# Performance work log

Hardware: AMD Instinct MI355X
Metric: run time of the kernel (lower is better)

Reference implementation:

```python
import jax, jax.numpy as jnp
import numpy as np

B, T, H, E = 256, 256, 512, 96  # batch, enc seq len, hidden/enc dim, charset size


def setup_inputs() -> dict:
    key = jax.random.key(0)
    ks = jax.random.split(key, 9)
    s = 0.05  # param scale
    return {
        "prev_h": jax.random.normal(ks[0], (B, H), jnp.float32),
        "prev_c": jax.random.normal(ks[1], (B, H), jnp.float32),
        "batch_H": jax.random.normal(ks[2], (B, T, H), jnp.float32),
        "char_onehots": jax.nn.one_hot(jax.random.randint(ks[3], (B,), 0, E), E, dtype=jnp.float32),
        "W_i2h": jax.random.normal(ks[4], (H, H), jnp.float32) * s,
        "W_h2h": jax.random.normal(ks[5], (H, H), jnp.float32) * s,
        "b_h2h": jnp.zeros((H,), jnp.float32),
        "w_score": jax.random.normal(ks[6], (H, 1), jnp.float32) * s,
        "W_lstm": jax.random.normal(ks[7], (H + E, 4 * H), jnp.float32) * s,
        "U_lstm": jax.random.normal(ks[8], (H, 4 * H), jnp.float32) * s,
        "b_lstm": jnp.zeros((4 * H,), jnp.float32),
    }


def reference(prev_h, prev_c, batch_H, char_onehots,
              W_i2h, W_h2h, b_h2h, w_score, W_lstm, U_lstm, b_lstm):
    # Additive (Bahdanau) attention
    proj = jnp.einsum('btd,dh->bth', batch_H, W_i2h)          # [B,T,H]
    hp = prev_h @ W_h2h + b_h2h                               # [B,H]
    e = jnp.tanh(proj + hp[:, None, :]) @ w_score             # [B,T,1]
    alpha = jax.nn.softmax(e, axis=1)                         # [B,T,1]
    context = jnp.einsum('bt,btd->bd', alpha[..., 0], batch_H)  # [B,D]
    x = jnp.concatenate([context, char_onehots], axis=1)      # [B,D+E]
    # Keras LSTMCell: gate order i, f, c(g), o
    z = x @ W_lstm + prev_h @ U_lstm + b_lstm                 # [B,4H]
    i, f, g, o = jnp.split(z, 4, axis=1)
    c_new = jax.nn.sigmoid(f) * prev_c + jax.nn.sigmoid(i) * jnp.tanh(g)
    h_new = jax.nn.sigmoid(o) * jnp.tanh(c_new)
    return h_new, c_new, alpha
```

## Files before the change

kernel.cpp:

```cpp
#include <hip/hip_runtime.h>
#include <hip/hip_bf16.h>
#include <math.h>

#define Bq 256
#define Tq 256
#define Hq 512
#define Eq 96

typedef __attribute__((ext_vector_type(8))) short short8;
typedef __attribute__((ext_vector_type(4))) float f32x4;

static __device__ __forceinline__ unsigned short f2bf(float f) {
  union { float f; unsigned u; } v; v.f = f;
  unsigned r = v.u + 0x7FFF + ((v.u >> 16) & 1);
  return (unsigned short)(r >> 16);
}

static __device__ __forceinline__ ushort4 pack4(float4 v) {
  ushort4 p;
  p.x = f2bf(v.x); p.y = f2bf(v.y); p.z = f2bf(v.z); p.w = f2bf(v.w);
  return p;
}

static __device__ __forceinline__ float sat_tanh(float x) {
  float ax = fminf(fabsf(x), 15.0f);
  float e = __builtin_exp2f(ax * 2.885390082f);
  float t = 1.0f - 2.0f / (e + 1.0f);
  return copysignf(t, x);
}

static __device__ __forceinline__ float sat_sig(float x) {
  float cx = fmaxf(fminf(x, 30.0f), -30.0f);
  return 1.0f / (1.0f + __builtin_exp2f(-cx * 1.442695041f));
}

__global__ __launch_bounds__(256) void convW_k(const float* __restrict__ W,
                                               unsigned short* __restrict__ Wt) {
  __shared__ float tile[32][33];
  int bx = blockIdx.x & 15, by = blockIdx.x >> 4;
  int tx = threadIdx.x & 31, ty = threadIdx.x >> 5;
  #pragma unroll
  for (int i = 0; i < 32; i += 8)
    tile[ty + i][tx] = W[(size_t)(by * 32 + ty + i) * Hq + bx * 32 + tx];
  __syncthreads();
  #pragma unroll
  for (int i = 0; i < 32; i += 8)
    Wt[(size_t)(bx * 32 + ty + i) * Hq + by * 32 + tx] = f2bf(tile[tx][ty + i]);
}

__global__ __launch_bounds__(256) void hsplit_k(const float* __restrict__ ph,
                                                const float* __restrict__ Whh,
                                                float* __restrict__ hp) {
  __shared__ __align__(16) float xs[8][128];
  const int ks = blockIdx.x & 3;
  const int nc = (blockIdx.x >> 2) & 3;
  const int bg = blockIdx.x >> 4;
  const int tid = threadIdx.x;
  const int row0 = bg * 8;
  const int d0 = ks * 128;
  for (int i = tid; i < 8 * 32; i += 256) {
    int r = i >> 5, dd = (i & 31) * 4;
    *(float4*)&xs[r][dd] = *(const float4*)&ph[(size_t)(row0 + r) * Hq + d0 + dd];
  }
  __syncthreads();
  const int rt = tid >> 6;
  const int ct = tid & 63;
  const int n = nc * 128 + ct * 2;
  float a00 = 0, a01 = 0, a10 = 0, a11 = 0;
  for (int dd = 0; dd < 128; dd += 4) {
    float4 x0 = *(const float4*)&xs[rt * 2][dd];
    float4 x1 = *(const float4*)&xs[rt * 2 + 1][dd];
    #pragma unroll
    for (int j = 0; j < 4; j++) {
      float2 w = *(const float2*)&Whh[(size_t)(d0 + dd + j) * Hq + n];
      float xj0 = ((const float*)&x0)[j];
      float xj1 = ((const float*)&x1)[j];
      a00 += xj0 * w.x; a01 += xj0 * w.y;
      a10 += xj1 * w.x; a11 += xj1 * w.y;
    }
  }
  int row = row0 + rt * 2;
  atomicAdd(&hp[(size_t)row * Hq + n], a00);
  atomicAdd(&hp[(size_t)row * Hq + n + 1], a01);
  atomicAdd(&hp[(size_t)(row + 1) * Hq + n], a10);
  atomicAdd(&hp[(size_t)(row + 1) * Hq + n + 1], a11);
}

#define LDKA 520

__global__ __launch_bounds__(512, 2) void fused_score3_k(
    const float* __restrict__ A,
    const unsigned short* __restrict__ Wt,
    const float* __restrict__ hp,
    const float* __restrict__ bh,
    const float* __restrict__ wsc,
    float* __restrict__ e) {
  __shared__ unsigned short As[64 * LDKA];
  __shared__ float red[8][64];

  const int tid = threadIdx.x;
  const int m0 = blockIdx.x * 64;
  const int b = m0 >> 8;
  const int wave = tid >> 6;
  const int lane = tid & 63;
  const int quad = lane >> 4;
  const int l16 = lane & 15;
  const int wn = wave * 64;

  {
    const int sr = tid >> 3;
    const int sc = (tid & 7) * 64;
    const float* Ar = A + (size_t)(m0 + sr) * Hq + sc;
    unsigned short* dst = &As[sr * LDKA + sc];
    #pragma unroll
    for (int j = 0; j < 64; j += 8) {
      float4 v0 = *(const float4*)&Ar[j];
      float4 v1 = *(const float4*)&Ar[j + 4];
      *(ushort4*)&dst[j] = pack4(v0);
      *(ushort4*)&dst[j + 4] = pack4(v1);
    }
  }
  __syncthreads();

  f32x4 acc[4][4] = {};
  const unsigned short* Bp = Wt + (size_t)(wn + l16) * Hq + quad * 8;
  const unsigned short* Ap = &As[l16 * LDKA + quad * 8];

  #pragma unroll 4
  for (int ks = 0; ks < 16; ks++) {
    const int k0 = ks * 32;
    short8 af[4];
    #pragma unroll
    for (int mi = 0; mi < 4; mi++)
      af[mi] = *(const short8*)(Ap + mi * 16 * LDKA + k0);
    #pragma unroll
    for (int ni = 0; ni < 4; ni++) {
      short8 bf = *(const short8*)(Bp + (size_t)ni * 16 * Hq + k0);
      #pragma unroll
      for (int mi = 0; mi < 4; mi++)
        acc[mi][ni] = __builtin_amdgcn_mfma_f32_16x16x32_bf16(
            af[mi], bf, acc[mi][ni], 0, 0, 0);
    }
  }

  float hv[4], wv[4];
  #pragma unroll
  for (int ni = 0; ni < 4; ni++) {
    int c = wn + ni * 16 + l16;
    hv[ni] = hp[(size_t)b * Hq + c] + bh[c];
    wv[ni] = wsc[c];
  }
  #pragma unroll
  for (int mi = 0; mi < 4; mi++) {
    float s[4] = {0, 0, 0, 0};
    #pragma unroll
    for (int ni = 0; ni < 4; ni++)
      #pragma unroll
      for (int r = 0; r < 4; r++)
        s[r] += sat_tanh(acc[mi][ni][r] + hv[ni]) * wv[ni];
    #pragma unroll
    for (int r = 0; r < 4; r++) {
      s[r] += __shfl_xor(s[r], 8, 64);
      s[r] += __shfl_xor(s[r], 4, 64);
      s[r] += __shfl_xor(s[r], 2, 64);
      s[r] += __shfl_xor(s[r], 1, 64);
    }
    if (l16 == 0) {
      #pragma unroll
      for (int r = 0; r < 4; r++) red[wave][mi * 16 + quad * 4 + r] = s[r];
    }
  }
  __syncthreads();
  if (tid < 64) {
    float t = 0.f;
    #pragma unroll
    for (int w = 0; w < 8; w++) t += red[w][tid];
    e[m0 + tid] = t;
  }
}

__global__ __launch_bounds__(256) void softmax_k(float* __restrict__ ea) {
  __shared__ float red[8];
  int b = blockIdx.x, t = threadIdx.x;
  int wave = t >> 6, lane = t & 63;
  float x = ea[b * Tq + t];
  float m = x;
  #pragma unroll
  for (int off = 32; off >= 1; off >>= 1) m = fmaxf(m, __shfl_xor(m, off, 64));
  if (lane == 0) red[wave] = m;
  __syncthreads();
  m = fmaxf(fmaxf(red[0], red[1]), fmaxf(red[2], red[3]));
  float ex = __builtin_exp2f((x - m) * 1.442695041f);
  float s = ex;
  #pragma unroll
  for (int off = 32; off >= 1; off >>= 1) s += __shfl_xor(s, off, 64);
  if (lane == 0) red[4 + wave] = s;
  __syncthreads();
  s = red[4] + red[5] + red[6] + red[7];
  ea[b * Tq + t] = ex / s;
}

__global__ __launch_bounds__(256) void ctxsplit_k(const float* __restrict__ alpha,
                                                  const float* __restrict__ bH,
                                                  float* __restrict__ ctx) {
  __shared__ float al[64];
  const int b = blockIdx.x >> 2;
  const int tc = blockIdx.x & 3;
  const int tid = threadIdx.x;
  if (tid < 64) al[tid] = alpha[b * Tq + tc * 64 + tid];
  __syncthreads();
  const float2* Hp = (const float2*)(bH + (size_t)b * Tq * Hq + (size_t)tc * 64 * Hq);
  float ax = 0.f, ay = 0.f;
  #pragma unroll 8
  for (int t = 0; t < 64; t++) {
    float a = al[t];
    float2 v = Hp[t * (Hq / 2) + tid];
    ax += a * v.x;
    ay += a * v.y;
  }
  atomicAdd(&ctx[(size_t)b * Hq + 2 * tid], ax);
  atomicAdd(&ctx[(size_t)b * Hq + 2 * tid + 1], ay);
}

__global__ __launch_bounds__(256) void zsplit_k(
    const float* __restrict__ ctx, const float* __restrict__ oneh,
    const float* __restrict__ ph, const float* __restrict__ Wl,
    const float* __restrict__ Ul, float* __restrict__ z) {
  __shared__ __align__(16) float xs[8 * 280];
  const int ks = blockIdx.x & 3;
  const int hc = (blockIdx.x >> 2) & 7;
  const int bg = blockIdx.x >> 5;
  const int tid = threadIdx.x;
  const int row0 = bg * 8;
  const int dbase = ks * 280;

  for (int i = tid; i < 8 * 280; i += 256) {
    int r = i / 280, dd = i % 280;
    int g = dbase + dd;
    float v;
    if (g < 512) v = ctx[(size_t)(row0 + r) * Hq + g];
    else if (g < 608) v = oneh[(row0 + r) * Eq + (g - 512)];
    else v = ph[(size_t)(row0 + r) * Hq + (g - 608)];
    xs[r * 280 + dd] = v;
  }
  __syncthreads();

  const int rt = tid >> 6;
  const int ct = tid & 63;
  const int c0 = ct * 4;
  const int gate = c0 >> 6;
  const int ho = c0 & 63;
  const int n = gate * 512 + hc * 64 + ho;

  float acc0[4] = {0, 0, 0, 0};
  float acc1[4] = {0, 0, 0, 0};
  const float* xr0 = &xs[(rt * 2) * 280];
  const float* xr1 = &xs[(rt * 2 + 1) * 280];

  for (int dd = 0; dd < 280; dd += 4) {
    float4 x0 = *(const float4*)&xr0[dd];
    float4 x1 = *(const float4*)&xr1[dd];
    #pragma unroll
    for (int j = 0; j < 4; j++) {
      int d = dbase + dd + j;
      const float* wp = (d < 608) ? &Wl[(size_t)d * 2048 + n]
                                  : &Ul[(size_t)(d - 608) * 2048 + n];
      float4 w = *(const float4*)wp;
      float a = ((const float*)&x0)[j], b = ((const float*)&x1)[j];
      acc0[0] += a * w.x; acc0[1] += a * w.y; acc0[2] += a * w.z; acc0[3] += a * w.w;
      acc1[0] += b * w.x; acc1[1] += b * w.y; acc1[2] += b * w.z; acc1[3] += b * w.w;
    }
  }
  const int r0 = row0 + rt * 2;
  #pragma unroll
  for (int j = 0; j < 4; j++) {
    atomicAdd(&z[(size_t)r0 * 2048 + n + j], acc0[j]);
    atomicAdd(&z[(size_t)(r0 + 1) * 2048 + n + j], acc1[j]);
  }
}

__global__ __launch_bounds__(256) void gatesz_k(const float* __restrict__ z,
                                                const float* __restrict__ bl,
                                                const float* __restrict__ pc,
                                                float* __restrict__ outh,
                                                float* __restrict__ outc) {
  int p = blockIdx.x * 256 + threadIdx.x;
  #pragma unroll
  for (int q = 0; q < 2; q++, p += 65536) {
    int r = p >> 9, h = p & 511;
    const float* zb = z + (size_t)r * 2048;
    float gi = zb[h] + bl[h];
    float gf = zb[512 + h] + bl[512 + h];
    float gg = zb[1024 + h] + bl[1024 + h];
    float go = zb[1536 + h] + bl[1536 + h];
    float cn = sat_sig(gf) * pc[p] + sat_sig(gi) * sat_tanh(gg);
    float hn = sat_sig(go) * sat_tanh(cn);
    outh[p] = hn;
    outc[p] = cn;
  }
}

#define KXc 1120
__global__ __launch_bounds__(256) void zgates2_k(
    const float* __restrict__ ctx, const float* __restrict__ oneh,
    const float* __restrict__ ph, const float* __restrict__ pc,
    const float* __restrict__ Wl, const float* __restrict__ Ul,
    const float* __restrict__ bl,
    float* __restrict__ outh, float* __restrict__ outc) {
  __shared__ __align__(16) float xs[8 * KXc];
  const int bg = blockIdx.x >> 3;
  const int hc = blockIdx.x & 7;
  const int tid = threadIdx.x;
  const int row0 = bg * 8;

  for (int i = tid; i < 8 * 128; i += 256) {
    int r = i >> 7, dd = (i & 127) * 4;
    *(float4*)&xs[r * KXc + dd] = *(const float4*)&ctx[(size_t)(row0 + r) * Hq + dd];
  }
  for (int i = tid; i < 8 * 128; i += 256) {
    int r = i >> 7, dd = (i & 127) * 4;
    *(float4*)&xs[r * KXc + 608 + dd] = *(const float4*)&ph[(size_t)(row0 + r) * Hq + dd];
  }
  if (tid < 8 * 24) {
    int r = tid / 24, dd = (tid % 24) * 4;
    *(float4*)&xs[r * KXc + 512 + dd] = *(const float4*)&oneh[(row0 + r) * Eq + dd];
  }
  __syncthreads();

  const int rt = tid >> 6;
  const int ct = tid & 63;
  const int c0 = ct * 4;
  const int gate = c0 >> 6;
  const int ho = c0 & 63;
  const int n = gate * 512 + hc * 64 + ho;

  float acc0[4] = {0, 0, 0, 0};
  float acc1[4] = {0, 0, 0, 0};
  const float* xr0 = &xs[(rt * 2) * KXc];
  const float* xr1 = &xs[(rt * 2 + 1) * KXc];

  for (int d = 0; d < 608; d += 4) {
    float4 x0 = *(const float4*)&xr0[d];
    float4 x1 = *(const float4*)&xr1[d];
    #pragma unroll
    for (int j = 0; j < 4; j++) {
      float4 w = *(const float4*)&Wl[(size_t)(d + j) * 2048 + n];
      float a = ((const float*)&x0)[j], b = ((const float*)&x1)[j];
      acc0[0] += a * w.x; acc0[1] += a * w.y; acc0[2] += a * w.z; acc0[3] += a * w.w;
      acc1[0] += b * w.x; acc1[1] += b * w.y; acc1[2] += b * w.z; acc1[3] += b * w.w;
    }
  }
  for (int d = 0; d < 512; d += 4) {
    float4 x0 = *(const float4*)&xr0[608 + d];
    float4 x1 = *(const float4*)&xr1[608 + d];
    #pragma unroll
    for (int j = 0; j < 4; j++) {
      float4 w = *(const float4*)&Ul[(size_t)(d + j) * 2048 + n];
      float a = ((const float*)&x0)[j], b = ((const float*)&x1)[j];
      acc0[0] += a * w.x; acc0[1] += a * w.y; acc0[2] += a * w.z; acc0[3] += a * w.w;
      acc1[0] += b * w.x; acc1[1] += b * w.y; acc1[2] += b * w.z; acc1[3] += b * w.w;
    }
  }

  __syncthreads();
  float* zs = xs;
  #pragma unroll
  for (int j = 0; j < 4; j++) {
    zs[(rt * 2) * 256 + c0 + j] = acc0[j];
    zs[(rt * 2 + 1) * 256 + c0 + j] = acc1[j];
  }
  __syncthreads();

  #pragma unroll
  for (int p = tid; p < 512; p += 256) {
    int r = p >> 6, o = p & 63;
    int h = hc * 64 + o;
    int grow = row0 + r;
    float gi = zs[r * 256 + o]       + bl[h];
    float gf = zs[r * 256 + 64 + o]  + bl[512 + h];
    float gg = zs[r * 256 + 128 + o] + bl[1024 + h];
    float go = zs[r * 256 + 192 + o] + bl[1536 + h];
    float cn = sat_sig(gf) * pc[(size_t)grow * Hq + h] + sat_sig(gi) * sat_tanh(gg);
    float hn = sat_sig(go) * sat_tanh(cn);
    outh[(size_t)grow * Hq + h] = hn;
    outc[(size_t)grow * Hq + h] = cn;
  }
}

extern "C" void kernel_launch(void* const* d_in, const int* in_sizes, int n_in,
                              void* d_out, int out_size, void* d_ws, size_t ws_size,
                              hipStream_t stream) {
  const float* prev_h = (const float*)d_in[0];
  const float* prev_c = (const float*)d_in[1];
  const float* batch_H = (const float*)d_in[2];
  const float* oneh = (const float*)d_in[3];
  const float* W_i2h = (const float*)d_in[4];
  const float* W_h2h = (const float*)d_in[5];
  const float* b_h2h = (const float*)d_in[6];
  const float* w_score = (const float*)d_in[7];
  const float* W_lstm = (const float*)d_in[8];
  const float* U_lstm = (const float*)d_in[9];
  const float* b_lstm = (const float*)d_in[10];

  float* out = (float*)d_out;
  float* outh = out;
  float* outc = out + Bq * Hq;
  float* alpha = out + 2 * Bq * Hq;

  float* ws = (float*)d_ws;
  float* hp = ws;
  float* ctx = ws;
  unsigned short* Wt = (unsigned short*)(ws + 131072);
  float* z = ws + 131072;

  const bool bigws = ws_size >= 2621440;

  hipMemsetAsync(hp, 0, Bq * Hq * sizeof(float), stream);
  convW_k<<<256, 256, 0, stream>>>(W_i2h, Wt);
  hsplit_k<<<512, 256, 0, stream>>>(prev_h, W_h2h, hp);
  fused_score3_k<<<1024, 512, 0, stream>>>(batch_H, Wt, hp, b_h2h, w_score, alpha);
  softmax_k<<<256, 256, 0, stream>>>(alpha);
  if (bigws) {
    hipMemsetAsync(ws, 0, 2621440, stream);
    ctxsplit_k<<<1024, 256, 0, stream>>>(alpha, batch_H, ctx);
    zsplit_k<<<1024, 256, 0, stream>>>(ctx, oneh, prev_h, W_lstm, U_lstm, z);
    gatesz_k<<<256, 256, 0, stream>>>(z, b_lstm, prev_c, outh, outc);
  } else {
    hipMemsetAsync(ctx, 0, Bq * Hq * sizeof(float), stream);
    ctxsplit_k<<<1024, 256, 0, stream>>>(alpha, batch_H, ctx);
    zgates2_k<<<256, 256, 0, stream>>>(ctx, oneh, prev_h, prev_c,
                                       W_lstm, U_lstm, b_lstm, outh, outc);
  }
}
```

Baseline: 403.1 us.

## Retile attention score GEMM with double-buffered LDS tiles and enlarge zsplit row tiles

The score GEMM moves from 64-row blocks that read Wt straight from global memory to 128x256 tiles. Both A and Wt are staged through double-buffered LDS with 32-wide k-steps, and the next tile is prefetched while MFMAs run. Because each block now covers half of the N dimension, partial scores are combined with atomicAdd into alpha, which now needs a memset first. ctxsplit switches to float4 loads with a split over time steps, and zsplit processes 32 rows per block with 4 rows per thread, reusing each loaded weight vector across more rows. The costs are more atomics, an extra memset, and more block syncs.

```diff
diff --git a/kernel.cpp b/kernel.cpp
--- a/kernel.cpp
+++ b/kernel.cpp
@@ -86,67 +86,82 @@
   atomicAdd(&hp[(size_t)(row + 1) * Hq + n + 1], a11);
 }
 
-#define LDKA 520
-
-__global__ __launch_bounds__(512, 2) void fused_score3_k(
+#define LDK4 40
+
+__global__ __launch_bounds__(1024, 4) void fused_score4_k(
     const float* __restrict__ A,
     const unsigned short* __restrict__ Wt,
     const float* __restrict__ hp,
     const float* __restrict__ bh,
     const float* __restrict__ wsc,
     float* __restrict__ e) {
-  __shared__ unsigned short As[64 * LDKA];
-  __shared__ float red[8][64];
+  __shared__ unsigned short As[2][128 * LDK4];
+  __shared__ unsigned short Bs[2][256 * LDK4];
+  __shared__ float red[8][128];
 
   const int tid = threadIdx.x;
-  const int m0 = blockIdx.x * 64;
+  const int n0 = blockIdx.x * 256;
+  const int m0 = blockIdx.y * 128;
   const int b = m0 >> 8;
   const int wave = tid >> 6;
   const int lane = tid & 63;
   const int quad = lane >> 4;
   const int l16 = lane & 15;
-  const int wn = wave * 64;
+  const int wm = wave >> 3;
+  const int wn8 = wave & 7;
+
+  const int ar = tid >> 3, ac = (tid & 7) * 4;
+  const int bc = tid >> 2, bk = (tid & 3) * 8;
+  const float* Agp = A + (size_t)(m0 + ar) * Hq + ac;
+  const unsigned short* Bgp = Wt + (size_t)(n0 + bc) * Hq + bk;
+
+  f32x4 acc[4][2] = {};
 
   {
-    const int sr = tid >> 3;
-    const int sc = (tid & 7) * 64;
-    const float* Ar = A + (size_t)(m0 + sr) * Hq + sc;
-    unsigned short* dst = &As[sr * LDKA + sc];
-    #pragma unroll
-    for (int j = 0; j < 64; j += 8) {
-      float4 v0 = *(const float4*)&Ar[j];
-      float4 v1 = *(const float4*)&Ar[j + 4];
-      *(ushort4*)&dst[j] = pack4(v0);
-      *(ushort4*)&dst[j + 4] = pack4(v1);
-    }
-  }
-  __syncthreads();
-
-  f32x4 acc[4][4] = {};
-  const unsigned short* Bp = Wt + (size_t)(wn + l16) * Hq + quad * 8;
-  const unsigned short* Ap = &As[l16 * LDKA + quad * 8];
-
-  #pragma unroll 4
+    float4 a0 = *(const float4*)Agp;
+    uint4 b0 = *(const uint4*)Bgp;
+    *(ushort4*)&As[0][ar * LDK4 + ac] = pack4(a0);
+    *(uint4*)&Bs[0][bc * LDK4 + bk] = b0;
+  }
+  __syncthreads();
+
+  int cur = 0;
+  #pragma unroll 2
   for (int ks = 0; ks < 16; ks++) {
-    const int k0 = ks * 32;
-    short8 af[4];
+    float4 an;
+    uint4 bn;
+    if (ks < 15) {
+      an = *(const float4*)(Agp + (ks + 1) * 32);
+      bn = *(const uint4*)(Bgp + (ks + 1) * 32);
+    }
+
+    short8 af[4], bf[2];
     #pragma unroll
     for (int mi = 0; mi < 4; mi++)
-      af[mi] = *(const short8*)(Ap + mi * 16 * LDKA + k0);
-    #pragma unroll
-    for (int ni = 0; ni < 4; ni++) {
-      short8 bf = *(const short8*)(Bp + (size_t)ni * 16 * Hq + k0);
+      af[mi] = *(const short8*)&As[cur][(wm * 64 + mi * 16 + l16) * LDK4 + quad * 8];
+    #pragma unroll
+    for (int ni = 0; ni < 2; ni++)
+      bf[ni] = *(const short8*)&Bs[cur][(wn8 * 32 + ni * 16 + l16) * LDK4 + quad * 8];
+
+    #pragma unroll
+    for (int mi = 0; mi < 4; mi++)
       #pragma unroll
-      for (int mi = 0; mi < 4; mi++)
+      for (int ni = 0; ni < 2; ni++)
         acc[mi][ni] = __builtin_amdgcn_mfma_f32_16x16x32_bf16(
-            af[mi], bf, acc[mi][ni], 0, 0, 0);
-    }
-  }
-
-  float hv[4], wv[4];
-  #pragma unroll
-  for (int ni = 0; ni < 4; ni++) {
-    int c = wn + ni * 16 + l16;
+            af[mi], bf[ni], acc[mi][ni], 0, 0, 0);
+
+    if (ks < 15) {
+      *(ushort4*)&As[cur ^ 1][ar * LDK4 + ac] = pack4(an);
+      *(uint4*)&Bs[cur ^ 1][bc * LDK4 + bk] = bn;
+    }
+    __syncthreads();
+    cur ^= 1;
+  }
+
+  float hv[2], wv[2];
+  #pragma unroll
+  for (int ni = 0; ni < 2; ni++) {
+    int c = n0 + wn8 * 32 + ni * 16 + l16;
     hv[ni] = hp[(size_t)b * Hq + c] + bh[c];
     wv[ni] = wsc[c];
   }
@@ -154,7 +169,7 @@
   for (int mi = 0; mi < 4; mi++) {
     float s[4] = {0, 0, 0, 0};
     #pragma unroll
-    for (int ni = 0; ni < 4; ni++)
+    for (int ni = 0; ni < 2; ni++)
       #pragma unroll
       for (int r = 0; r < 4; r++)
         s[r] += sat_tanh(acc[mi][ni][r] + hv[ni]) * wv[ni];
@@ -167,15 +182,16 @@
     }
     if (l16 == 0) {
       #pragma unroll
-      for (int r = 0; r < 4; r++) red[wave][mi * 16 + quad * 4 + r] = s[r];
-    }
-  }
-  __syncthreads();
-  if (tid < 64) {
+      for (int r = 0; r < 4; r++)
+        red[wn8][wm * 64 + mi * 16 + quad * 4 + r] = s[r];
+    }
+  }
+  __syncthreads();
+  if (tid < 128) {
     float t = 0.f;
     #pragma unroll
-    for (int w = 0; w < 8; w++) t += red[w][tid];
-    e[m0 + tid] = t;
+    for (int w8 = 0; w8 < 8; w8++) t += red[w8][tid];
+    atomicAdd(&e[m0 + tid], t);
   }
 }
 
@@ -209,32 +225,36 @@
   const int tid = threadIdx.x;
   if (tid < 64) al[tid] = alpha[b * Tq + tc * 64 + tid];
   __syncthreads();
-  const float2* Hp = (const float2*)(bH + (size_t)b * Tq * Hq + (size_t)tc * 64 * Hq);
-  float ax = 0.f, ay = 0.f;
+  const float* Hp = bH + (size_t)b * Tq * Hq + (size_t)tc * 64 * Hq;
+  const int h4 = (tid & 127) * 4;
+  const int t0 = (tid >> 7) * 32;
+  float a0 = 0.f, a1 = 0.f, a2 = 0.f, a3 = 0.f;
   #pragma unroll 8
-  for (int t = 0; t < 64; t++) {
-    float a = al[t];
-    float2 v = Hp[t * (Hq / 2) + tid];
-    ax += a * v.x;
-    ay += a * v.y;
-  }
-  atomicAdd(&ctx[(size_t)b * Hq + 2 * tid], ax);
-  atomicAdd(&ctx[(size_t)b * Hq + 2 * tid + 1], ay);
-}
-
-__global__ __launch_bounds__(256) void zsplit_k(
+  for (int t = 0; t < 32; t++) {
+    float a = al[t0 + t];
+    float4 v = *(const float4*)&Hp[(size_t)(t0 + t) * Hq + h4];
+    a0 += a * v.x; a1 += a * v.y; a2 += a * v.z; a3 += a * v.w;
+  }
+  float* cp = &ctx[(size_t)b * Hq + h4];
+  atomicAdd(cp + 0, a0);
+  atomicAdd(cp + 1, a1);
+  atomicAdd(cp + 2, a2);
+  atomicAdd(cp + 3, a3);
+}
+
+__global__ __launch_bounds__(512) void zsplit_k(
     const float* __restrict__ ctx, const float* __restrict__ oneh,
     const float* __restrict__ ph, const float* __restrict__ Wl,
     const float* __restrict__ Ul, float* __restrict__ z) {
-  __shared__ __align__(16) float xs[8 * 280];
+  __shared__ float xs[32 * 280];
   const int ks = blockIdx.x & 3;
   const int hc = (blockIdx.x >> 2) & 7;
   const int bg = blockIdx.x >> 5;
   const int tid = threadIdx.x;
-  const int row0 = bg * 8;
+  const int row0 = bg * 32;
   const int dbase = ks * 280;
 
-  for (int i = tid; i < 8 * 280; i += 256) {
+  for (int i = tid; i < 32 * 280; i += 512) {
     int r = i / 280, dd = i % 280;
     int g = dbase + dd;
     float v;
@@ -252,30 +272,25 @@
   const int ho = c0 & 63;
   const int n = gate * 512 + hc * 64 + ho;
 
-  float acc0[4] = {0, 0, 0, 0};
-  float acc1[4] = {0, 0, 0, 0};
-  const float* xr0 = &xs[(rt * 2) * 280];
-  const float* xr1 = &xs[(rt * 2 + 1) * 280];
-
-  for (int dd = 0; dd < 280; dd += 4) {
-    float4 x0 = *(const float4*)&xr0[dd];
-    float4 x1 = *(const float4*)&xr1[dd];
-    #pragma unroll
-    for (int j = 0; j < 4; j++) {
-      int d = dbase + dd + j;
-      const float* wp = (d < 608) ? &Wl[(size_t)d * 2048 + n]
-                                  : &Ul[(size_t)(d - 608) * 2048 + n];
-      float4 w = *(const float4*)wp;
-      float a = ((const float*)&x0)[j], b = ((const float*)&x1)[j];
-      acc0[0] += a * w.x; acc0[1] += a * w.y; acc0[2] += a * w.z; acc0[3] += a * w.w;
-      acc1[0] += b * w.x; acc1[1] += b * w.y; acc1[2] += b * w.z; acc1[3] += b * w.w;
-    }
-  }
-  const int r0 = row0 + rt * 2;
-  #pragma unroll
-  for (int j = 0; j < 4; j++) {
-    atomicAdd(&z[(size_t)r0 * 2048 + n + j], acc0[j]);
-    atomicAdd(&z[(size_t)(r0 + 1) * 2048 + n + j], acc1[j]);
+  float acc[4][4] = {};
+  #pragma unroll 4
+  for (int dd = 0; dd < 280; dd++) {
+    int g = dbase + dd;
+    const float* wp = (g < 608) ? &Wl[(size_t)g * 2048 + n]
+                                : &Ul[(size_t)(g - 608) * 2048 + n];
+    float4 w = *(const float4*)wp;
+    #pragma unroll
+    for (int r = 0; r < 4; r++) {
+      float x = xs[(rt * 4 + r) * 280 + dd];
+      acc[r][0] += x * w.x; acc[r][1] += x * w.y;
+      acc[r][2] += x * w.z; acc[r][3] += x * w.w;
+    }
+  }
+  #pragma unroll
+  for (int r = 0; r < 4; r++) {
+    float* zp = &z[(size_t)(row0 + rt * 4 + r) * 2048 + n];
+    #pragma unroll
+    for (int j = 0; j < 4; j++) atomicAdd(zp + j, acc[r][j]);
   }
 }
 
@@ -415,15 +430,17 @@
 
   const bool bigws = ws_size >= 2621440;
 
+  hipMemsetAsync(alpha, 0, Bq * Tq * sizeof(float), stream);
   hipMemsetAsync(hp, 0, Bq * Hq * sizeof(float), stream);
   convW_k<<<256, 256, 0, stream>>>(W_i2h, Wt);
   hsplit_k<<<512, 256, 0, stream>>>(prev_h, W_h2h, hp);
-  fused_score3_k<<<1024, 512, 0, stream>>>(batch_H, Wt, hp, b_h2h, w_score, alpha);
+  dim3 g4(2, 512);
+  fused_score4_k<<<g4, 1024, 0, stream>>>(batch_H, Wt, hp, b_h2h, w_score, alpha);
   softmax_k<<<256, 256, 0, stream>>>(alpha);
   if (bigws) {
     hipMemsetAsync(ws, 0, 2621440, stream);
     ctxsplit_k<<<1024, 256, 0, stream>>>(alpha, batch_H, ctx);
-    zsplit_k<<<1024, 256, 0, stream>>>(ctx, oneh, prev_h, W_lstm, U_lstm, z);
+    zsplit_k<<<256, 512, 0, stream>>>(ctx, oneh, prev_h, W_lstm, U_lstm, z);
     gatesz_k<<<256, 256, 0, stream>>>(z, b_lstm, prev_c, outh, outc);
   } else {
     hipMemsetAsync(ctx, 0, Bq * Hq * sizeof(float), stream);
```

After: 435.2 us. 7.9% more time.

## Retile score GEMM into double-buffered 128x128 tiles and widen zsplit rows

Applied to the files above, without the earlier changes.

The attention score kernel now uses a 2D grid of 128x128 output tiles. A and B are staged through double-buffered shared memory with 64-wide K steps, and the next K slice is prefetched while the current one runs on MFMA. Partial scores across the four N tiles are combined with atomicAdd into a pre-zeroed alpha buffer, which needs an extra memset. The LSTM z kernel now computes 8 rows per thread instead of 2, so each weight load is reused more and the grid shrinks fourfold, at the cost of more registers and shared memory.

```diff
diff --git a/kernel.cpp b/kernel.cpp
--- a/kernel.cpp
+++ b/kernel.cpp
@@ -20,6 +20,12 @@
   ushort4 p;
   p.x = f2bf(v.x); p.y = f2bf(v.y); p.z = f2bf(v.z); p.w = f2bf(v.w);
   return p;
+}
+
+static __device__ __forceinline__ short8 pack8(float4 a, float4 b) {
+  union { short8 s; ushort4 u[2]; } r;
+  r.u[0] = pack4(a); r.u[1] = pack4(b);
+  return r.s;
 }
 
 static __device__ __forceinline__ float sat_tanh(float x) {
@@ -86,67 +92,95 @@
   atomicAdd(&hp[(size_t)(row + 1) * Hq + n + 1], a11);
 }
 
-#define LDKA 520
-
-__global__ __launch_bounds__(512, 2) void fused_score3_k(
+#define LDKA 72
+
+__global__ __launch_bounds__(512) void fused_score5_k(
     const float* __restrict__ A,
     const unsigned short* __restrict__ Wt,
     const float* __restrict__ hp,
     const float* __restrict__ bh,
     const float* __restrict__ wsc,
     float* __restrict__ e) {
-  __shared__ unsigned short As[64 * LDKA];
+  __shared__ unsigned short As[2][128 * LDKA];
+  __shared__ unsigned short Bs[2][128 * LDKA];
   __shared__ float red[8][64];
 
   const int tid = threadIdx.x;
-  const int m0 = blockIdx.x * 64;
+  const int n0 = blockIdx.x * 128;
+  const int m0 = blockIdx.y * 128;
   const int b = m0 >> 8;
   const int wave = tid >> 6;
   const int lane = tid & 63;
   const int quad = lane >> 4;
   const int l16 = lane & 15;
-  const int wn = wave * 64;
+  const int wm = wave >> 2;
+  const int wn4 = wave & 3;
+
+  const int arow = tid >> 2, aq = tid & 3;
+  const float* Agp = A + (size_t)(m0 + arow) * Hq + aq * 16;
+  const unsigned short* Bgp = Wt + (size_t)(n0 + arow) * Hq + aq * 16;
+
+  f32x4 acc[4][2] = {};
 
   {
-    const int sr = tid >> 3;
-    const int sc = (tid & 7) * 64;
-    const float* Ar = A + (size_t)(m0 + sr) * Hq + sc;
-    unsigned short* dst = &As[sr * LDKA + sc];
-    #pragma unroll
-    for (int j = 0; j < 64; j += 8) {
-      float4 v0 = *(const float4*)&Ar[j];
-      float4 v1 = *(const float4*)&Ar[j + 4];
-      *(ushort4*)&dst[j] = pack4(v0);
-      *(ushort4*)&dst[j + 4] = pack4(v1);
-    }
-  }
-  __syncthreads();
-
-  f32x4 acc[4][4] = {};
-  const unsigned short* Bp = Wt + (size_t)(wn + l16) * Hq + quad * 8;
-  const unsigned short* Ap = &As[l16 * LDKA + quad * 8];
-
-  #pragma unroll 4
-  for (int ks = 0; ks < 16; ks++) {
-    const int k0 = ks * 32;
-    short8 af[4];
+    float4 a0[4]; uint4 b0[2];
+    #pragma unroll
+    for (int q = 0; q < 4; q++) a0[q] = *(const float4*)(Agp + q * 4);
+    b0[0] = *(const uint4*)(Bgp);
+    b0[1] = *(const uint4*)(Bgp + 8);
+    *(short8*)&As[0][arow * LDKA + aq * 16] = pack8(a0[0], a0[1]);
+    *(short8*)&As[0][arow * LDKA + aq * 16 + 8] = pack8(a0[2], a0[3]);
+    *(uint4*)&Bs[0][arow * LDKA + aq * 16] = b0[0];
+    *(uint4*)&Bs[0][arow * LDKA + aq * 16 + 8] = b0[1];
+  }
+  __syncthreads();
+
+  int cur = 0;
+  for (int ks = 0; ks < 8; ks++) {
+    float4 aN[4]; uint4 bN[2];
+    if (ks < 7) {
+      const int k1 = (ks + 1) * 64;
+      #pragma unroll
+      for (int q = 0; q < 4; q++) aN[q] = *(const float4*)(Agp + k1 + q * 4);
+      bN[0] = *(const uint4*)(Bgp + k1);
+      bN[1] = *(const uint4*)(Bgp + k1 + 8);
+    }
+
+    short8 af[4][2], bf[2][2];
     #pragma unroll
     for (int mi = 0; mi < 4; mi++)
-      af[mi] = *(const short8*)(Ap + mi * 16 * LDKA + k0);
-    #pragma unroll
-    for (int ni = 0; ni < 4; ni++) {
-      short8 bf = *(const short8*)(Bp + (size_t)ni * 16 * Hq + k0);
+      #pragma unroll
+      for (int k2 = 0; k2 < 2; k2++)
+        af[mi][k2] = *(const short8*)&As[cur][(wm * 64 + mi * 16 + l16) * LDKA + k2 * 32 + quad * 8];
+    #pragma unroll
+    for (int ni = 0; ni < 2; ni++)
+      #pragma unroll
+      for (int k2 = 0; k2 < 2; k2++)
+        bf[ni][k2] = *(const short8*)&Bs[cur][(wn4 * 32 + ni * 16 + l16) * LDKA + k2 * 32 + quad * 8];
+
+    #pragma unroll
+    for (int k2 = 0; k2 < 2; k2++)
       #pragma unroll
       for (int mi = 0; mi < 4; mi++)
-        acc[mi][ni] = __builtin_amdgcn_mfma_f32_16x16x32_bf16(
-            af[mi], bf, acc[mi][ni], 0, 0, 0);
-    }
-  }
-
-  float hv[4], wv[4];
-  #pragma unroll
-  for (int ni = 0; ni < 4; ni++) {
-    int c = wn + ni * 16 + l16;
+        #pragma unroll
+        for (int ni = 0; ni < 2; ni++)
+          acc[mi][ni] = __builtin_amdgcn_mfma_f32_16x16x32_bf16(
+              af[mi][k2], bf[ni][k2], acc[mi][ni], 0, 0, 0);
+
+    if (ks < 7) {
+      *(short8*)&As[cur ^ 1][arow * LDKA + aq * 16] = pack8(aN[0], aN[1]);
+      *(short8*)&As[cur ^ 1][arow * LDKA + aq * 16 + 8] = pack8(aN[2], aN[3]);
+      *(uint4*)&Bs[cur ^ 1][arow * LDKA + aq * 16] = bN[0];
+      *(uint4*)&Bs[cur ^ 1][arow * LDKA + aq * 16 + 8] = bN[1];
+    }
+    __syncthreads();
+    cur ^= 1;
+  }
+
+  float hv[2], wv[2];
+  #pragma unroll
+  for (int ni = 0; ni < 2; ni++) {
+    int c = n0 + wn4 * 32 + ni * 16 + l16;
     hv[ni] = hp[(size_t)b * Hq + c] + bh[c];
     wv[ni] = wsc[c];
   }
@@ -154,7 +188,7 @@
   for (int mi = 0; mi < 4; mi++) {
     float s[4] = {0, 0, 0, 0};
     #pragma unroll
-    for (int ni = 0; ni < 4; ni++)
+    for (int ni = 0; ni < 2; ni++)
       #pragma unroll
       for (int r = 0; r < 4; r++)
         s[r] += sat_tanh(acc[mi][ni][r] + hv[ni]) * wv[ni];
@@ -171,11 +205,11 @@
     }
   }
   __syncthreads();
-  if (tid < 64) {
-    float t = 0.f;
-    #pragma unroll
-    for (int w = 0; w < 8; w++) t += red[w][tid];
-    e[m0 + tid] = t;
+  if (tid < 128) {
+    const int half = tid >> 6, ri = tid & 63;
+    float t = red[half * 4 + 0][ri] + red[half * 4 + 1][ri] +
+              red[half * 4 + 2][ri] + red[half * 4 + 3][ri];
+    atomicAdd(&e[m0 + tid], t);
   }
 }
 
@@ -226,15 +260,15 @@
     const float* __restrict__ ctx, const float* __restrict__ oneh,
     const float* __restrict__ ph, const float* __restrict__ Wl,
     const float* __restrict__ Ul, float* __restrict__ z) {
-  __shared__ __align__(16) float xs[8 * 280];
+  __shared__ __align__(16) float xs[32 * 280];
   const int ks = blockIdx.x & 3;
   const int hc = (blockIdx.x >> 2) & 7;
   const int bg = blockIdx.x >> 5;
   const int tid = threadIdx.x;
-  const int row0 = bg * 8;
+  const int row0 = bg * 32;
   const int dbase = ks * 280;
 
-  for (int i = tid; i < 8 * 280; i += 256) {
+  for (int i = tid; i < 32 * 280; i += 256) {
     int r = i / 280, dd = i % 280;
     int g = dbase + dd;
     float v;
@@ -252,30 +286,31 @@
   const int ho = c0 & 63;
   const int n = gate * 512 + hc * 64 + ho;
 
-  float acc0[4] = {0, 0, 0, 0};
-  float acc1[4] = {0, 0, 0, 0};
-  const float* xr0 = &xs[(rt * 2) * 280];
-  const float* xr1 = &xs[(rt * 2 + 1) * 280];
-
+  float acc[8][4] = {};
   for (int dd = 0; dd < 280; dd += 4) {
-    float4 x0 = *(const float4*)&xr0[dd];
-    float4 x1 = *(const float4*)&xr1[dd];
+    float4 xr[8];
+    #pragma unroll
+    for (int r = 0; r < 8; r++)
+      xr[r] = *(const float4*)&xs[(rt * 8 + r) * 280 + dd];
     #pragma unroll
     for (int j = 0; j < 4; j++) {
-      int d = dbase + dd + j;
-      const float* wp = (d < 608) ? &Wl[(size_t)d * 2048 + n]
-                                  : &Ul[(size_t)(d - 608) * 2048 + n];
+      int g = dbase + dd + j;
+      const float* wp = (g < 608) ? &Wl[(size_t)g * 2048 + n]
+                                  : &Ul[(size_t)(g - 608) * 2048 + n];
       float4 w = *(const float4*)wp;
-      float a = ((const float*)&x0)[j], b = ((const float*)&x1)[j];
-      acc0[0] += a * w.x; acc0[1] += a * w.y; acc0[2] += a * w.z; acc0[3] += a * w.w;
-      acc1[0] += b * w.x; acc1[1] += b * w.y; acc1[2] += b * w.z; acc1[3] += b * w.w;
-    }
-  }
-  const int r0 = row0 + rt * 2;
-  #pragma unroll
-  for (int j = 0; j < 4; j++) {
-    atomicAdd(&z[(size_t)r0 * 2048 + n + j], acc0[j]);
-    atomicAdd(&z[(size_t)(r0 + 1) * 2048 + n + j], acc1[j]);
+      #pragma unroll
+      for (int r = 0; r < 8; r++) {
+        float x = ((const float*)&xr[r])[j];
+        acc[r][0] += x * w.x; acc[r][1] += x * w.y;
+        acc[r][2] += x * w.z; acc[r][3] += x * w.w;
+      }
+    }
+  }
+  #pragma unroll
+  for (int r = 0; r < 8; r++) {
+    float* zp = &z[(size_t)(row0 + rt * 8 + r) * 2048 + n];
+    #pragma unroll
+    for (int j = 0; j < 4; j++) atomicAdd(zp + j, acc[r][j]);
   }
 }
 
@@ -415,15 +450,17 @@
 
   const bool bigws = ws_size >= 2621440;
 
+  hipMemsetAsync(alpha, 0, Bq * Tq * sizeof(float), stream);
   hipMemsetAsync(hp, 0, Bq * Hq * sizeof(float), stream);
   convW_k<<<256, 256, 0, stream>>>(W_i2h, Wt);
   hsplit_k<<<512, 256, 0, stream>>>(prev_h, W_h2h, hp);
-  fused_score3_k<<<1024, 512, 0, stream>>>(batch_H, Wt, hp, b_h2h, w_score, alpha);
+  dim3 g5(4, 512);
+  fused_score5_k<<<g5, 512, 0, stream>>>(batch_H, Wt, hp, b_h2h, w_score, alpha);
   softmax_k<<<256, 256, 0, stream>>>(alpha);
   if (bigws) {
     hipMemsetAsync(ws, 0, 2621440, stream);
     ctxsplit_k<<<1024, 256, 0, stream>>>(alpha, batch_H, ctx);
-    zsplit_k<<<1024, 256, 0, stream>>>(ctx, oneh, prev_h, W_lstm, U_lstm, z);
+    zsplit_k<<<256, 256, 0, stream>>>(ctx, oneh, prev_h, W_lstm, U_lstm, z);
     gatesz_k<<<256, 256, 0, stream>>>(z, b_lstm, prev_c, outh, outc);
   } else {
     hipMemsetAsync(ctx, 0, Bq * Hq * sizeof(float), stream);
```

After: 407.4 us. About the same (+1.0%).
